# Performance work log

Measured on AMD Instinct MI355X. Metric: run time of the kernel, lower is better.

## Reference

```python
import jax, jax.numpy as jnp
import numpy as np

EMB_DIM = 2048
N_Q_HEADS = 32
N_KV_HEADS = 8
HEAD_DIM = EMB_DIM // N_Q_HEADS  # 64
N_REP = N_Q_HEADS // N_KV_HEADS  # 4
ROPE_BASE = 10000.0


def setup_inputs() -> dict:
    key = jax.random.key(0)
    ks = jax.random.split(key, 9)
    B, T = 2, 2048
    kv_dim = HEAD_DIM * N_KV_HEADS
    s = 0.02
    return {
        "x":  jax.random.normal(ks[0], (B, T, EMB_DIM), jnp.float32),
        "Wq": jax.random.normal(ks[1], (EMB_DIM, EMB_DIM), jnp.float32) * s,
        "bq": jax.random.normal(ks[2], (EMB_DIM,), jnp.float32) * s,
        "Wk": jax.random.normal(ks[3], (kv_dim, EMB_DIM), jnp.float32) * s,
        "bk": jax.random.normal(ks[4], (kv_dim,), jnp.float32) * s,
        "Wv": jax.random.normal(ks[5], (kv_dim, EMB_DIM), jnp.float32) * s,
        "bv": jax.random.normal(ks[6], (kv_dim,), jnp.float32) * s,
        "Wo": jax.random.normal(ks[7], (EMB_DIM, EMB_DIM), jnp.float32) * s,
        "bo": jax.random.normal(ks[8], (EMB_DIM,), jnp.float32) * s,
    }


def _rope_tables(T, D, dtype):
    inv_freq = 1.0 / (ROPE_BASE ** (jnp.arange(0, D, 2, dtype=jnp.float32) / D))
    t = jnp.arange(T, dtype=jnp.float32)
    freqs = jnp.einsum("i,j->ij", t, inv_freq)          # [T, D/2]
    emb = jnp.concatenate([freqs, freqs], axis=-1)       # [T, D]
    # broadcast over batch and heads: [1, T, 1, D]
    return jnp.cos(emb)[None, :, None, :].astype(dtype), jnp.sin(emb)[None, :, None, :].astype(dtype)


def _rotate_half(x):
    x1, x2 = jnp.split(x, 2, axis=-1)
    return jnp.concatenate([-x2, x1], axis=-1)


def reference(x, Wq, bq, Wk, bk, Wv, bv, Wo, bo):
    B, T, C = x.shape
    q = (x @ Wq.T + bq).reshape(B, T, N_Q_HEADS, HEAD_DIM)
    k = (x @ Wk.T + bk).reshape(B, T, N_KV_HEADS, HEAD_DIM)
    v = (x @ Wv.T + bv).reshape(B, T, N_KV_HEADS, HEAD_DIM)

    cos, sin = _rope_tables(T, HEAD_DIM, x.dtype)
    q = q * cos + _rotate_half(q) * sin
    k = k * cos + _rotate_half(k) * sin

    q = q.transpose(0, 2, 1, 3)                          # [B, Hq, T, D]
    k = k.transpose(0, 2, 1, 3)                          # [B, Hkv, T, D]
    v = v.transpose(0, 2, 1, 3)
    # GQA: repeat_interleave kv heads to match query heads
    k = jnp.repeat(k, N_REP, axis=1)                     # [B, Hq, T, D]
    v = jnp.repeat(v, N_REP, axis=1)

    scale = 1.0 / jnp.sqrt(jnp.asarray(HEAD_DIM, x.dtype))
    att = jnp.einsum("bhqd,bhkd->bhqk", q, k) * scale    # [B, Hq, T, T]
    causal = jnp.tril(jnp.ones((T, T), dtype=bool))
    att = jnp.where(causal[None, None], att, -jnp.inf)
    att = jax.nn.softmax(att, axis=-1)

    y = jnp.einsum("bhqk,bhkd->bhqd", att, v)            # [B, Hq, T, D]
    y = y.transpose(0, 2, 1, 3).reshape(B, T, C)
    return y @ Wo.T + bo
```

## Files before the change

kernel.cpp:

```cpp
#include <hip/hip_runtime.h>
#include <hip/hip_bf16.h>
#include <math.h>


typedef __attribute__((ext_vector_type(8))) short short8;
typedef __attribute__((ext_vector_type(4))) float f32x4;
typedef __attribute__((ext_vector_type(16))) float f32x16;
typedef __attribute__((ext_vector_type(2))) unsigned int uint2v;

#define MFMA16(a,b,c) __builtin_amdgcn_mfma_f32_16x16x32_bf16((a),(b),(c),0,0,0)
#define MFMA32(a,b,c) __builtin_amdgcn_mfma_f32_32x32x16_bf16((a),(b),(c),0,0,0)
#define QSCALE 0.18033688011112043f
#define NFREQ  (-13.28771237954945f / 32.0f)

__device__ __forceinline__ ushort f2bf(float f) {
  union { float f; unsigned u; } x; x.f = f;
  unsigned r = x.u + 0x7fffu + ((x.u >> 16) & 1u);
  return (ushort)(r >> 16);
}
__device__ __forceinline__ uint pkbf(float a, float b) {
  union { float f; unsigned u; } x, y; x.f = a; y.f = b;
  return ((x.u + 0x8000u) >> 16) | ((y.u + 0x8000u) & 0xffff0000u);
}

__device__ __forceinline__ void g2l16(const void* g, void* l) {
  __builtin_amdgcn_global_load_lds(
      (__attribute__((address_space(1))) void*)g,
      (__attribute__((address_space(3))) void*)l, 16, 0, 0);
}

__global__ void cvt_all(const float* __restrict__ x,  const float* __restrict__ wq,
                        const float* __restrict__ wk, const float* __restrict__ wv,
                        const float* __restrict__ wo,
                        ushort* __restrict__ x_bf, ushort* __restrict__ wqkv,
                        ushort* __restrict__ wo_bf) {
  int i = blockIdx.x * 256 + threadIdx.x;
  const float4* src; ushort* dst; int off;
  if (i < 2097152)      { src = (const float4*)x;  dst = x_bf;             off = i; }
  else if (i < 3145728) { src = (const float4*)wq; dst = wqkv;             off = i - 2097152; }
  else if (i < 3407872) { src = (const float4*)wk; dst = wqkv + 4194304;   off = i - 3145728; }
  else if (i < 3670016) { src = (const float4*)wv; dst = wqkv + 5242880;   off = i - 3407872; }
  else                  { src = (const float4*)wo; dst = wo_bf;            off = i - 3670016; }
  float4 v = src[off];
  ushort4 o;
  o.x = f2bf(v.x); o.y = f2bf(v.y); o.z = f2bf(v.z); o.w = f2bf(v.w);
  ((ushort4*)dst)[off] = o;
}

__global__ __launch_bounds__(256, 3)
void gemm_qkv(const ushort* __restrict__ A, const ushort* __restrict__ Bw,
              const float* __restrict__ bq, const float* __restrict__ bk,
              const float* __restrict__ bv,
              ushort* __restrict__ qr, ushort* __restrict__ kr,
              ushort* __restrict__ vt) {
  const int K = 2048;
  __shared__ ushort As[2][128*32];
  __shared__ ushort Bs[2][128*32];
  const int tid = threadIdx.x;
  const int wave = tid >> 6, lane = tid & 63;
  const int wm = wave >> 1, wn = wave & 1;
  const int quad = lane >> 4, l16 = lane & 15;
  const int swg = (l16 >> 1) & 3;
  int id = blockIdx.y * 24 + blockIdx.x;
  id = (id & 7) * 96 + (id >> 3);
  const int bx = id % 24, by = id / 24;
  const int m0 = by * 128, n0 = bx * 128;

  f32x4 acc[4][4] = {};

  auto stage = [&](int buf, int k0) {
#pragma unroll
    for (int i = 0; i < 2; ++i) {
      int cbase = (i*4 + wave) * 64;
      int p = cbase + lane;
      int row = p >> 2, pcb = p & 3;
      int cl = pcb ^ ((row >> 1) & 3);
      g2l16(A  + (size_t)(m0 + row) * K + k0 + cl * 8, As[buf] + (size_t)cbase * 8);
      g2l16(Bw + (size_t)(n0 + row) * K + k0 + cl * 8, Bs[buf] + (size_t)cbase * 8);
    }
  };

  stage(0, 0);
  for (int k0 = 0; k0 < K; k0 += 32) {
    __syncthreads();
    int cur = (k0 >> 5) & 1;
    if (k0 + 32 < K) stage(cur ^ 1, k0 + 32);

    short8 af[4], bfr[4];
#pragma unroll
    for (int mi = 0; mi < 4; ++mi)
      af[mi] = *(const short8*)(As[cur] + (wm*64 + mi*16 + l16)*32 + ((quad ^ swg) * 8));
#pragma unroll
    for (int ni = 0; ni < 4; ++ni)
      bfr[ni] = *(const short8*)(Bs[cur] + (wn*64 + ni*16 + l16)*32 + ((quad ^ swg) * 8));
#pragma unroll
    for (int mi = 0; mi < 4; ++mi)
#pragma unroll
      for (int ni = 0; ni < 4; ++ni)
        acc[mi][ni] = MFMA16(af[mi], bfr[ni], acc[mi][ni]);
  }

  const int bb = m0 >> 11;
  const int tb = (m0 & 2047) + wm*64;

  if (bx < 20) {
    const bool isq = bx < 16;
    const float scale = isq ? QSCALE : 1.0f;
#pragma unroll
    for (int ni = 0; ni < 2; ++ni) {
      int n = n0 + wn*64 + ni*16 + l16;
      int d = ni*16 + l16;
      float bias1, bias2;
      ushort* dst;
      if (isq) {
        bias1 = bq[n]; bias2 = bq[n + 32];
        dst = qr + ((size_t)(bb*32 + (n >> 6)) * 2048) * 64 + d;
      } else {
        bias1 = bk[n - 2048]; bias2 = bk[n - 2016];
        dst = kr + ((size_t)(bb*8 + ((n >> 6) - 32)) * 2048) * 64 + d;
      }
      float invf = exp2f((float)d * NFREQ);
#pragma unroll
      for (int mi = 0; mi < 4; ++mi) {
#pragma unroll
        for (int r = 0; r < 4; ++r) {
          int t = tb + mi*16 + quad*4 + r;
          float x1 = acc[mi][ni][r]   + bias1;
          float x2 = acc[mi][ni+2][r] + bias2;
          float f = (float)t * invf;
          float sn = __sinf(f), cs = __cosf(f);
          dst[(size_t)t*64]      = f2bf((x1*cs - x2*sn) * scale);
          dst[(size_t)t*64 + 32] = f2bf((x2*cs + x1*sn) * scale);
        }
      }
    }
  } else {
#pragma unroll
    for (int ni = 0; ni < 4; ++ni) {
      int n = n0 + wn*64 + ni*16 + l16;
      int d = ni*16 + l16;
      float bias = bv[n - 2560];
      ushort* dst = vt + ((size_t)(bb*8 + ((n - 2560) >> 6)) * 64 + d) * 2048;
#pragma unroll
      for (int mi = 0; mi < 4; ++mi) {
        int t = tb + mi*16 + quad*4;
        uint2 pk;
        pk.x = (uint)f2bf(acc[mi][ni][0]+bias) | ((uint)f2bf(acc[mi][ni][1]+bias) << 16);
        pk.y = (uint)f2bf(acc[mi][ni][2]+bias) | ((uint)f2bf(acc[mi][ni][3]+bias) << 16);
        *(uint2*)(dst + t) = pk;
      }
    }
  }
}

__global__ __launch_bounds__(256, 3)
void gemm128(const ushort* __restrict__ A, const ushort* __restrict__ Bw,
             const float* __restrict__ b0,
             float* __restrict__ Cout, int M, int N, int K) {
  __shared__ ushort As[2][128*32];
  __shared__ ushort Bs[2][128*32];
  const int tid = threadIdx.x;
  const int wave = tid >> 6, lane = tid & 63;
  const int wm = wave >> 1, wn = wave & 1;
  const int quad = lane >> 4, l16 = lane & 15;
  const int swg = (l16 >> 1) & 3;
  int id = blockIdx.y * 16 + blockIdx.x;
  id = (id & 7) * 64 + (id >> 3);
  const int m0 = (id / 16) * 128, n0 = (id % 16) * 128;

  f32x4 acc[4][4] = {};

  auto stage = [&](int buf, int k0) {
#pragma unroll
    for (int i = 0; i < 2; ++i) {
      int cbase = (i*4 + wave) * 64;
      int p = cbase + lane;
      int row = p >> 2, pcb = p & 3;
      int cl = pcb ^ ((row >> 1) & 3);
      g2l16(A  + (size_t)(m0 + row) * K + k0 + cl * 8, As[buf] + (size_t)cbase * 8);
      g2l16(Bw + (size_t)(n0 + row) * K + k0 + cl * 8, Bs[buf] + (size_t)cbase * 8);
    }
  };

  stage(0, 0);
  for (int k0 = 0; k0 < K; k0 += 32) {
    __syncthreads();
    int cur = (k0 >> 5) & 1;
    if (k0 + 32 < K) stage(cur ^ 1, k0 + 32);

    short8 af[4], bfr[4];
#pragma unroll
    for (int mi = 0; mi < 4; ++mi)
      af[mi] = *(const short8*)(As[cur] + (wm*64 + mi*16 + l16)*32 + ((quad ^ swg) * 8));
#pragma unroll
    for (int ni = 0; ni < 4; ++ni)
      bfr[ni] = *(const short8*)(Bs[cur] + (wn*64 + ni*16 + l16)*32 + ((quad ^ swg) * 8));
#pragma unroll
    for (int mi = 0; mi < 4; ++mi)
#pragma unroll
      for (int ni = 0; ni < 4; ++ni)
        acc[mi][ni] = MFMA16(af[mi], bfr[ni], acc[mi][ni]);
  }

#pragma unroll
  for (int ni = 0; ni < 4; ++ni) {
    int n = n0 + wn*64 + ni*16 + l16;
    float bias = b0[n];
#pragma unroll
    for (int mi = 0; mi < 4; ++mi) {
#pragma unroll
      for (int r = 0; r < 4; ++r) {
        int m = m0 + wm*64 + mi*16 + quad*4 + r;
        Cout[(size_t)m * N + n] = acc[mi][ni][r] + bias;
      }
    }
  }
}

__global__ __launch_bounds__(256, 2)
void attn(const ushort* __restrict__ Q, const ushort* __restrict__ Kb,
          const ushort* __restrict__ Vt, ushort* __restrict__ Y) {
  __shared__ ushort Ks[2][64*64];
  __shared__ ushort Vs[2][64*64];
  const int tid = threadIdx.x, wave = tid >> 6, lane = tid & 63;
  const int l32 = lane & 31, hh = lane >> 5;
  const int h = blockIdx.y, b = blockIdx.z;
  const int hk = h >> 2;
  const ushort* Qb = Q  + ((size_t)(b*32 + h)  * 2048) * 64;
  const ushort* Kg = Kb + ((size_t)(b*8 + hk) * 2048) * 64;
  const ushort* Vg = Vt + ((size_t)(b*8 + hk) * 64) * 2048;

  auto stage = [&](int buf, int kt) {
#pragma unroll
    for (int i = 0; i < 2; ++i) {
      int p = i*256 + tid;
      int row = p >> 3, pcb = p & 7;
      int cl = pcb ^ (row & 7);
      g2l16(Kg + (size_t)(kt*64 + row)*64 + cl*8, Ks[buf] + (size_t)p*8);
      g2l16(Vg + (size_t)row*2048 + kt*64 + cl*8, Vs[buf] + (size_t)p*8);
    }
  };

  for (int pass = 0; pass < 2; ++pass) {
    const int qt = pass ? (15 - blockIdx.x) : blockIdx.x;
    const int q0 = qt * 128;
    const int qrow = q0 + wave*32 + l32;
    short8 qf[4];
#pragma unroll
    for (int ks = 0; ks < 4; ++ks)
      qf[ks] = *(const short8*)(Qb + (size_t)qrow*64 + ks*16 + hh*8);

    f32x16 o[2] = {};
    float lsum = 0.f;

    __syncthreads();
    stage(0, 0);

    const int ktmax = qt*2 + 1;
    for (int kt = 0; kt <= ktmax; ++kt) {
      __syncthreads();
      int cur = kt & 1;
      if (kt < ktmax) stage(cur ^ 1, kt + 1);

      f32x16 s[2];
      __builtin_amdgcn_s_setprio(1);
#pragma unroll
      for (int kb = 0; kb < 2; ++kb) {
        f32x16 z = {};
#pragma unroll
        for (int ks = 0; ks < 4; ++ks) {
          int row = kb*32 + l32;
          short8 kf = *(const short8*)(Ks[cur] + row*64 + (((ks*2 + hh) ^ (row & 7)) * 8));
          z = MFMA32(kf, qf[ks], z);
        }
        s[kb] = z;
      }
      __builtin_amdgcn_s_setprio(0);

      if (kt*64 + 63 > qrow - l32) {
#pragma unroll
        for (int kb = 0; kb < 2; ++kb)
#pragma unroll
          for (int r = 0; r < 16; ++r) {
            int key = kt*64 + kb*32 + (r & 3) + 8*(r >> 2) + 4*hh;
            if (key > qrow) s[kb][r] = -INFINITY;
          }
      }

#pragma unroll
      for (int kb = 0; kb < 2; ++kb)
#pragma unroll
        for (int r = 0; r < 16; ++r) {
          s[kb][r] = __builtin_amdgcn_exp2f(s[kb][r]);
          lsum += s[kb][r];
        }

      __builtin_amdgcn_s_setprio(1);
#pragma unroll
      for (int kb = 0; kb < 2; ++kb) {
#pragma unroll
        for (int c = 0; c < 2; ++c) {
          int rb = c*8;
          uint a0 = pkbf(s[kb][rb+0], s[kb][rb+1]);
          uint b0 = pkbf(s[kb][rb+4], s[kb][rb+5]);
          uint a1 = pkbf(s[kb][rb+2], s[kb][rb+3]);
          uint b1 = pkbf(s[kb][rb+6], s[kb][rb+7]);
          uint2v r0 = __builtin_amdgcn_permlane32_swap(a0, b0, false, false);
          uint2v r1 = __builtin_amdgcn_permlane32_swap(a1, b1, false, false);
          union { uint u[4]; short8 s8; } pa;
          pa.u[0] = r0[0]; pa.u[1] = r1[0]; pa.u[2] = r0[1]; pa.u[3] = r1[1];
#pragma unroll
          for (int db = 0; db < 2; ++db) {
            int row = db*32 + l32;
            short8 vf = *(const short8*)(Vs[cur] + row*64 +
                          (((kb*4 + c*2 + hh) ^ (row & 7)) * 8));
            o[db] = MFMA32(vf, pa.s8, o[db]);
          }
        }
      }
      __builtin_amdgcn_s_setprio(0);
    }

    union { float f; uint u; } lu; lu.f = lsum;
    uint2v lr = __builtin_amdgcn_permlane32_swap(lu.u, lu.u, false, false);
    union { uint u; float f; } la, lb; la.u = lr[0]; lb.u = lr[1];
    float inv = 1.0f / (la.f + lb.f);

#pragma unroll
    for (int db = 0; db < 2; ++db) {
#pragma unroll
      for (int g = 0; g < 4; ++g) {
        int d = db*32 + 8*g + 4*hh;
        size_t base = ((size_t)(b*2048 + qrow)) * 2048 + h*64 + d;
        uint2 pk;
        pk.x = pkbf(o[db][4*g+0]*inv, o[db][4*g+1]*inv);
        pk.y = pkbf(o[db][4*g+2]*inv, o[db][4*g+3]*inv);
        *(uint2*)((ushort*)Y + base) = pk;
      }
    }
  }
}

extern "C" void kernel_launch(void* const* d_in, const int* in_sizes, int n_in,
                              void* d_out, int out_size, void* d_ws, size_t ws_size,
                              hipStream_t stream) {
  (void)in_sizes; (void)n_in; (void)out_size; (void)ws_size;
  const float* x  = (const float*)d_in[0];
  const float* Wq = (const float*)d_in[1];
  const float* bq = (const float*)d_in[2];
  const float* Wk = (const float*)d_in[3];
  const float* bk = (const float*)d_in[4];
  const float* Wv = (const float*)d_in[5];
  const float* bv = (const float*)d_in[6];
  const float* Wo = (const float*)d_in[7];
  const float* bo = (const float*)d_in[8];
  float* out = (float*)d_out;

  ushort* ws    = (ushort*)d_ws;
  ushort* x_bf  = ws;
  ushort* wqkv  = x_bf + 8388608;
  ushort* wo_bf = wqkv + 6291456;
  ushort* qr    = wo_bf + 4194304;
  ushort* kr    = qr + 8388608;
  ushort* vt    = kr + 2097152;
  ushort* Y     = x_bf;

  cvt_all<<<18432, 256, 0, stream>>>(x, Wq, Wk, Wv, Wo, x_bf, wqkv, wo_bf);
  gemm_qkv<<<dim3(24, 32), 256, 0, stream>>>(x_bf, wqkv, bq, bk, bv, qr, kr, vt);
  attn<<<dim3(8, 32, 2), 256, 0, stream>>>(qr, kr, vt, Y);
  gemm128<<<dim3(16, 32), 256, 0, stream>>>(Y, wo_bf, bo, out, 4096, 2048, 2048);
}
```

Baseline: 286.6 us.

## Split paired causal passes into separate blocks and raise attention occupancy

Each attention block used to handle two query tiles (qt and 15-qt) in sequence to balance causal work. Now the grid is doubled and each block handles one tile, with odd or even head groups taking mirrored tile order. The score loop processes one 32-key half at a time to lower register pressure, the band mask check is per wave, and launch bounds rise to 4 blocks per SM. This gives more parallel blocks and higher occupancy. The cost is unbalanced per-block work and each Q tile no longer being reused for its partner pass.

```diff
diff --git a/kernel.cpp b/kernel.cpp
--- a/kernel.cpp
+++ b/kernel.cpp
@@ -217,7 +217,7 @@
   }
 }
 
-__global__ __launch_bounds__(256, 2)
+__global__ __launch_bounds__(256, 4)
 void attn(const ushort* __restrict__ Q, const ushort* __restrict__ Kb,
           const ushort* __restrict__ Vt, ushort* __restrict__ Y) {
   __shared__ ushort Ks[2][64*64];
@@ -241,102 +241,92 @@
     }
   };
 
-  for (int pass = 0; pass < 2; ++pass) {
-    const int qt = pass ? (15 - blockIdx.x) : blockIdx.x;
-    const int q0 = qt * 128;
-    const int qrow = q0 + wave*32 + l32;
-    short8 qf[4];
-#pragma unroll
-    for (int ks = 0; ks < 4; ++ks)
-      qf[ks] = *(const short8*)(Qb + (size_t)qrow*64 + ks*16 + hh*8);
-
-    f32x16 o[2] = {};
-    float lsum = 0.f;
-
+  const int qt = (blockIdx.y & 16) ? (15 - blockIdx.x) : blockIdx.x;
+  const int q0 = qt * 128;
+  const int qrow = q0 + wave*32 + l32;
+  short8 qf[4];
+#pragma unroll
+  for (int ks = 0; ks < 4; ++ks)
+    qf[ks] = *(const short8*)(Qb + (size_t)qrow*64 + ks*16 + hh*8);
+
+  f32x16 o[2] = {};
+  float lsum = 0.f;
+
+  stage(0, 0);
+
+  const int ktmax = qt*2 + 1;
+  for (int kt = 0; kt <= ktmax; ++kt) {
     __syncthreads();
-    stage(0, 0);
-
-    const int ktmax = qt*2 + 1;
-    for (int kt = 0; kt <= ktmax; ++kt) {
-      __syncthreads();
-      int cur = kt & 1;
-      if (kt < ktmax) stage(cur ^ 1, kt + 1);
-
-      f32x16 s[2];
+    int cur = kt & 1;
+    if (kt < ktmax) stage(cur ^ 1, kt + 1);
+
+    const bool band = (kt*64 + 63 > q0 + wave*32);
+
+#pragma unroll
+    for (int kb = 0; kb < 2; ++kb) {
+      f32x16 s = {};
       __builtin_amdgcn_s_setprio(1);
 #pragma unroll
-      for (int kb = 0; kb < 2; ++kb) {
-        f32x16 z = {};
-#pragma unroll
-        for (int ks = 0; ks < 4; ++ks) {
-          int row = kb*32 + l32;
-          short8 kf = *(const short8*)(Ks[cur] + row*64 + (((ks*2 + hh) ^ (row & 7)) * 8));
-          z = MFMA32(kf, qf[ks], z);
+      for (int ks = 0; ks < 4; ++ks) {
+        int row = kb*32 + l32;
+        short8 kf = *(const short8*)(Ks[cur] + row*64 + (((ks*2 + hh) ^ (row & 7)) * 8));
+        s = MFMA32(kf, qf[ks], s);
+      }
+      __builtin_amdgcn_s_setprio(0);
+
+      if (band) {
+#pragma unroll
+        for (int r = 0; r < 16; ++r) {
+          int key = kt*64 + kb*32 + (r & 3) + 8*(r >> 2) + 4*hh;
+          if (key > qrow) s[r] = -INFINITY;
         }
-        s[kb] = z;
+      }
+
+#pragma unroll
+      for (int r = 0; r < 16; ++r) {
+        s[r] = __builtin_amdgcn_exp2f(s[r]);
+        lsum += s[r];
+      }
+
+      __builtin_amdgcn_s_setprio(1);
+#pragma unroll
+      for (int c = 0; c < 2; ++c) {
+        int rb = c*8;
+        uint a0 = pkbf(s[rb+0], s[rb+1]);
+        uint b0 = pkbf(s[rb+4], s[rb+5]);
+        uint a1 = pkbf(s[rb+2], s[rb+3]);
+        uint b1 = pkbf(s[rb+6], s[rb+7]);
+        uint2v r0 = __builtin_amdgcn_permlane32_swap(a0, b0, false, false);
+        uint2v r1 = __builtin_amdgcn_permlane32_swap(a1, b1, false, false);
+        union { uint u[4]; short8 s8; } pa;
+        pa.u[0] = r0[0]; pa.u[1] = r1[0]; pa.u[2] = r0[1]; pa.u[3] = r1[1];
+#pragma unroll
+        for (int db = 0; db < 2; ++db) {
+          int row = db*32 + l32;
+          short8 vf = *(const short8*)(Vs[cur] + row*64 +
+                        (((kb*4 + c*2 + hh) ^ (row & 7)) * 8));
+          o[db] = MFMA32(vf, pa.s8, o[db]);
+        }
       }
       __builtin_amdgcn_s_setprio(0);
-
-      if (kt*64 + 63 > qrow - l32) {
-#pragma unroll
-        for (int kb = 0; kb < 2; ++kb)
-#pragma unroll
-          for (int r = 0; r < 16; ++r) {
-            int key = kt*64 + kb*32 + (r & 3) + 8*(r >> 2) + 4*hh;
-            if (key > qrow) s[kb][r] = -INFINITY;
-          }
-      }
-
-#pragma unroll
-      for (int kb = 0; kb < 2; ++kb)
-#pragma unroll
-        for (int r = 0; r < 16; ++r) {
-          s[kb][r] = __builtin_amdgcn_exp2f(s[kb][r]);
-          lsum += s[kb][r];
-        }
-
-      __builtin_amdgcn_s_setprio(1);
-#pragma unroll
-      for (int kb = 0; kb < 2; ++kb) {
-#pragma unroll
-        for (int c = 0; c < 2; ++c) {
-          int rb = c*8;
-          uint a0 = pkbf(s[kb][rb+0], s[kb][rb+1]);
-          uint b0 = pkbf(s[kb][rb+4], s[kb][rb+5]);
-          uint a1 = pkbf(s[kb][rb+2], s[kb][rb+3]);
-          uint b1 = pkbf(s[kb][rb+6], s[kb][rb+7]);
-          uint2v r0 = __builtin_amdgcn_permlane32_swap(a0, b0, false, false);
-          uint2v r1 = __builtin_amdgcn_permlane32_swap(a1, b1, false, false);
-          union { uint u[4]; short8 s8; } pa;
-          pa.u[0] = r0[0]; pa.u[1] = r1[0]; pa.u[2] = r0[1]; pa.u[3] = r1[1];
-#pragma unroll
-          for (int db = 0; db < 2; ++db) {
-            int row = db*32 + l32;
-            short8 vf = *(const short8*)(Vs[cur] + row*64 +
-                          (((kb*4 + c*2 + hh) ^ (row & 7)) * 8));
-            o[db] = MFMA32(vf, pa.s8, o[db]);
-          }
-        }
-      }
-      __builtin_amdgcn_s_setprio(0);
-    }
-
-    union { float f; uint u; } lu; lu.f = lsum;
-    uint2v lr = __builtin_amdgcn_permlane32_swap(lu.u, lu.u, false, false);
-    union { uint u; float f; } la, lb; la.u = lr[0]; lb.u = lr[1];
-    float inv = 1.0f / (la.f + lb.f);
-
-#pragma unroll
-    for (int db = 0; db < 2; ++db) {
-#pragma unroll
-      for (int g = 0; g < 4; ++g) {
-        int d = db*32 + 8*g + 4*hh;
-        size_t base = ((size_t)(b*2048 + qrow)) * 2048 + h*64 + d;
-        uint2 pk;
-        pk.x = pkbf(o[db][4*g+0]*inv, o[db][4*g+1]*inv);
-        pk.y = pkbf(o[db][4*g+2]*inv, o[db][4*g+3]*inv);
-        *(uint2*)((ushort*)Y + base) = pk;
-      }
+    }
+  }
+
+  union { float f; uint u; } lu; lu.f = lsum;
+  uint2v lr = __builtin_amdgcn_permlane32_swap(lu.u, lu.u, false, false);
+  union { uint u; float f; } la, lb; la.u = lr[0]; lb.u = lr[1];
+  float inv = 1.0f / (la.f + lb.f);
+
+#pragma unroll
+  for (int db = 0; db < 2; ++db) {
+#pragma unroll
+    for (int g = 0; g < 4; ++g) {
+      int d = db*32 + 8*g + 4*hh;
+      size_t base = ((size_t)(b*2048 + qrow)) * 2048 + h*64 + d;
+      uint2 pk;
+      pk.x = pkbf(o[db][4*g+0]*inv, o[db][4*g+1]*inv);
+      pk.y = pkbf(o[db][4*g+2]*inv, o[db][4*g+3]*inv);
+      *(uint2*)((ushort*)Y + base) = pk;
     }
   }
 }
@@ -367,6 +357,6 @@
 
   cvt_all<<<18432, 256, 0, stream>>>(x, Wq, Wk, Wv, Wo, x_bf, wqkv, wo_bf);
   gemm_qkv<<<dim3(24, 32), 256, 0, stream>>>(x_bf, wqkv, bq, bk, bv, qr, kr, vt);
-  attn<<<dim3(8, 32, 2), 256, 0, stream>>>(qr, kr, vt, Y);
+  attn<<<dim3(16, 32, 2), 256, 0, stream>>>(qr, kr, vt, Y);
   gemm128<<<dim3(16, 32), 256, 0, stream>>>(Y, wo_bf, bo, out, 4096, 2048, 2048);
 }
```

New measurement: 294.4 us. +2.7%, slower.
